# Performance work log

Measured on AMD Instinct MI355X. Metric: run time of the kernel, lower is better.

The kernel has to match this reference:

```python
import jax, jax.numpy as jnp
import numpy as np

B, S, E = 8, 2048, 512
VOCAB, FVOCAB = 32000, 128
SCALE = float(np.power(E, 0.5))  # emb_size ** (0.5 * temper), temper=1


def setup_inputs() -> dict:
    key = jax.random.key(0)
    ks = jax.random.split(key, 7)
    key_seq = jax.random.randint(ks[0], (B, S), 0, VOCAB, dtype=jnp.int32)
    value_seq = jax.random.randint(ks[1], (B, S), 0, FVOCAB, dtype=jnp.int32)
    hidden = jax.random.normal(ks[2], (B, S, E), dtype=jnp.float32)
    mask_matrix = jax.random.uniform(ks[3], (B, S, S), dtype=jnp.float32)
    nan_matrix = jnp.zeros((1,), dtype=jnp.int32)  # unused by forward
    # learned params; padding_idx=0 -> zero row in embeddings
    key_emb = jax.random.normal(ks[4], (VOCAB, E), dtype=jnp.float32).at[0].set(0.0)
    value_emb = jax.random.normal(ks[5], (FVOCAB, E), dtype=jnp.float32).at[0].set(0.0)
    weight = jax.random.normal(ks[6], (E, E), dtype=jnp.float32) / np.sqrt(E)
    return {
        "key_seq": key_seq, "value_seq": value_seq, "hidden": hidden,
        "mask_matrix": mask_matrix, "nan_matrix": nan_matrix,
        "key_emb": key_emb, "value_emb": value_emb, "weight": weight,
    }


def reference(key_seq, value_seq, hidden, mask_matrix, nan_matrix,
              key_emb, value_emb, weight):
    k = key_emb[key_seq]          # [B,S,E]
    v = value_emb[value_seq]      # [B,S,E]
    q = jnp.einsum('bsd,de->bse', hidden, weight)   # hidden @ weight
    u = jnp.einsum('bse,bte->bst', q, k) / SCALE    # QK^T, [B,S,S]
    mask = jnp.clip(mask_matrix.astype(u.dtype), 0.0, 1.0)
    exp_u = jnp.exp(u)
    delta = exp_u * mask
    p = delta / (jnp.sum(delta, axis=2, keepdims=True) + 1e-10)
    o = jnp.einsum('bst,bte->bse', p, v)            # PV, [B,S,E]
    return o
```

## Files before the change

kernel.cpp:

```cpp
#include <hip/hip_runtime.h>
#include <stdint.h>

#define BB 8
#define SS 2048
#define EE 512
#define INV_SCALE 0.04419417382415922f

typedef __attribute__((ext_vector_type(8))) short bf8_t;
typedef __attribute__((ext_vector_type(4))) float f4_t;

__device__ __forceinline__ unsigned short f2bf(float f) {
    union { float f; uint32_t u; } x; x.f = f;
    uint32_t r = x.u + 0x7fffu + ((x.u >> 16) & 1u);
    return (unsigned short)(r >> 16);
}


__global__ void __launch_bounds__(256) gather_k_kernel(const int* __restrict__ idx,
                                                       const float* __restrict__ emb,
                                                       unsigned short* __restrict__ out) {
    int id = blockIdx.x * 256 + threadIdx.x;
    int chunk = id & 63;
    int row = id >> 6;
    int e0 = chunk * 8;
    int k = idx[row];
    const float* src = emb + (size_t)k * EE + e0;
    float4 a = *(const float4*)(src);
    float4 c = *(const float4*)(src + 4);
    union { unsigned short s[8]; int4 v; } u;
    u.s[0] = f2bf(a.x); u.s[1] = f2bf(a.y); u.s[2] = f2bf(a.z); u.s[3] = f2bf(a.w);
    u.s[4] = f2bf(c.x); u.s[5] = f2bf(c.y); u.s[6] = f2bf(c.z); u.s[7] = f2bf(c.w);
    *(int4*)(out + (size_t)row * EE + e0) = u.v;
}

__global__ void __launch_bounds__(256) cast_h_kernel(const float* __restrict__ in,
                                                     unsigned short* __restrict__ out) {
    int id = blockIdx.x * 256 + threadIdx.x;
    const float* src = in + (size_t)id * 8;
    float4 a = *(const float4*)(src);
    float4 c = *(const float4*)(src + 4);
    union { unsigned short s[8]; int4 v; } u;
    u.s[0] = f2bf(a.x); u.s[1] = f2bf(a.y); u.s[2] = f2bf(a.z); u.s[3] = f2bf(a.w);
    u.s[4] = f2bf(c.x); u.s[5] = f2bf(c.y); u.s[6] = f2bf(c.z); u.s[7] = f2bf(c.w);
    *(int4*)(out + (size_t)id * 8) = u.v;
}

__global__ void __launch_bounds__(256) gather_vt_kernel(const int* __restrict__ idx,
                                                        const float* __restrict__ emb,
                                                        unsigned short* __restrict__ vt) {
    int id = blockIdx.x * 256 + threadIdx.x;
    int t = id & (SS - 1);
    int rest = id >> 11;
    int e = rest & (EE - 1);
    int b = rest >> 9;
    int k = idx[b * SS + t];
    vt[id] = f2bf(emb[(size_t)k * EE + e]);
}

__global__ void __launch_bounds__(256) transpose_w_kernel(const float* __restrict__ w,
                                                          unsigned short* __restrict__ wt) {
    int id = blockIdx.x * 256 + threadIdx.x;
    int e = id & (EE - 1);
    int f = id >> 9;
    wt[id] = f2bf(w[(size_t)e * EE + f] * INV_SCALE);
}


__device__ __forceinline__ void stage_tile(const unsigned short* gbase, int ld, int k0,
                                           unsigned short* lds, int wave, int lane) {
#pragma unroll
    for (int i = 0; i < 2; ++i) {
        int row = i * 64 + wave * 16 + (lane >> 2);
        int col = (lane & 3) * 8;
        const unsigned short* g = gbase + (size_t)row * ld + (k0 + col);
        unsigned short* l = lds + i * 2048 + wave * 512 + lane * 8;
        __builtin_amdgcn_global_load_lds((const __attribute__((address_space(1))) unsigned int*)g,
                                         (__attribute__((address_space(3))) unsigned int*)l,
                                         16, 0, 0);
    }
}

template <int KLEN>
__device__ __forceinline__ void mfma_loop(const unsigned short* Abase, int lda,
                                          const unsigned short* Bbase, int ldb,
                                          unsigned short* As, unsigned short* Bs,
                                          f4_t acc[4][4], int wave, int lane) {
    const int wm = wave >> 1, wn = wave & 1;
    const int quad = lane >> 4, l16 = lane & 15;
#pragma unroll 1
    for (int k0 = 0; k0 < KLEN; k0 += 32) {
        stage_tile(Abase, lda, k0, As, wave, lane);
        stage_tile(Bbase, ldb, k0, Bs, wave, lane);
        __syncthreads();
        bf8_t af[4], bfr[4];
#pragma unroll
        for (int mi = 0; mi < 4; ++mi)
            af[mi] = *(const bf8_t*)(As + (wm * 64 + mi * 16 + l16) * 32 + quad * 8);
#pragma unroll
        for (int ni = 0; ni < 4; ++ni)
            bfr[ni] = *(const bf8_t*)(Bs + (wn * 64 + ni * 16 + l16) * 32 + quad * 8);
#pragma unroll
        for (int mi = 0; mi < 4; ++mi)
#pragma unroll
            for (int ni = 0; ni < 4; ++ni)
                acc[mi][ni] = __builtin_amdgcn_mfma_f32_16x16x32_bf16(af[mi], bfr[ni],
                                                                      acc[mi][ni], 0, 0, 0);
        __syncthreads();
    }
}


__global__ void __launch_bounds__(256) qgen_kernel(const unsigned short* __restrict__ H,
                                                   const unsigned short* __restrict__ Wt,
                                                   unsigned short* __restrict__ Q) {
    __shared__ unsigned short As[128 * 32];
    __shared__ unsigned short Bs[128 * 32];
    const int tid = threadIdx.x, wave = tid >> 6, lane = tid & 63;
    const int rowT = blockIdx.y;
    const int colT = blockIdx.x;
    f4_t acc[4][4];
    const f4_t z = {0.f, 0.f, 0.f, 0.f};
    for (int i = 0; i < 4; ++i) for (int j = 0; j < 4; ++j) acc[i][j] = z;
    mfma_loop<EE>(H + (size_t)rowT * 128 * EE, EE,
                  Wt + (size_t)colT * 128 * EE, EE, As, Bs, acc, wave, lane);
    const int wm = wave >> 1, wn = wave & 1, quad = lane >> 4, l16 = lane & 15;
#pragma unroll
    for (int mi = 0; mi < 4; ++mi)
#pragma unroll
        for (int r = 0; r < 4; ++r) {
            int row = rowT * 128 + wm * 64 + mi * 16 + quad * 4 + r;
#pragma unroll
            for (int ni = 0; ni < 4; ++ni) {
                int col = colT * 128 + wn * 64 + ni * 16 + l16;
                Q[(size_t)row * EE + col] = f2bf(acc[mi][ni][r]);
            }
        }
}

__global__ void __launch_bounds__(256) qk_kernel(const unsigned short* __restrict__ Q,
                                                 const unsigned short* __restrict__ K,
                                                 const float* __restrict__ mask,
                                                 unsigned short* __restrict__ delta,
                                                 float* __restrict__ lsum) {
    __shared__ unsigned short As[128 * 32];
    __shared__ unsigned short Bs[128 * 32];
    const int tid = threadIdx.x, wave = tid >> 6, lane = tid & 63;
    const int b = blockIdx.z, qT = blockIdx.y, tT = blockIdx.x;
    f4_t acc[4][4];
    const f4_t z = {0.f, 0.f, 0.f, 0.f};
    for (int i = 0; i < 4; ++i) for (int j = 0; j < 4; ++j) acc[i][j] = z;
    mfma_loop<EE>(Q + ((size_t)b * SS + qT * 128) * EE, EE,
                  K + ((size_t)b * SS + tT * 128) * EE, EE, As, Bs, acc, wave, lane);
    const int wm = wave >> 1, wn = wave & 1, quad = lane >> 4, l16 = lane & 15;
#pragma unroll
    for (int mi = 0; mi < 4; ++mi)
#pragma unroll
        for (int r = 0; r < 4; ++r) {
            int row = qT * 128 + wm * 64 + mi * 16 + quad * 4 + r;
            const float* mrow = mask + ((size_t)b * SS + row) * SS;
            unsigned short* drow = delta + ((size_t)b * SS + row) * SS;
            float psum = 0.f;
#pragma unroll
            for (int ni = 0; ni < 4; ++ni) {
                int col = tT * 128 + wn * 64 + ni * 16 + l16;
                float m = mrow[col];
                m = fminf(fmaxf(m, 0.f), 1.f);
                float e = __expf(acc[mi][ni][r]) * m;
                drow[col] = f2bf(e);
                psum += e;
            }
#pragma unroll
            for (int off = 1; off < 16; off <<= 1)
                psum += __shfl_xor(psum, off, 16);
            if (l16 == 0) atomicAdd(&lsum[b * SS + row], psum);
        }
}

__global__ void __launch_bounds__(256) pv_kernel(const unsigned short* __restrict__ delta,
                                                 const unsigned short* __restrict__ Vt,
                                                 const float* __restrict__ lsum,
                                                 float* __restrict__ out) {
    __shared__ unsigned short As[128 * 32];
    __shared__ unsigned short Bs[128 * 32];
    const int tid = threadIdx.x, wave = tid >> 6, lane = tid & 63;
    const int b = blockIdx.z, qT = blockIdx.y, eT = blockIdx.x;
    f4_t acc[4][4];
    const f4_t z = {0.f, 0.f, 0.f, 0.f};
    for (int i = 0; i < 4; ++i) for (int j = 0; j < 4; ++j) acc[i][j] = z;
    mfma_loop<SS>(delta + ((size_t)b * SS + qT * 128) * SS, SS,
                  Vt + ((size_t)b * EE + eT * 128) * SS, SS, As, Bs, acc, wave, lane);
    const int wm = wave >> 1, wn = wave & 1, quad = lane >> 4, l16 = lane & 15;
#pragma unroll
    for (int mi = 0; mi < 4; ++mi)
#pragma unroll
        for (int r = 0; r < 4; ++r) {
            int row = qT * 128 + wm * 64 + mi * 16 + quad * 4 + r;
            float inv = 1.0f / (lsum[b * SS + row] + 1e-10f);
#pragma unroll
            for (int ni = 0; ni < 4; ++ni) {
                int col = eT * 128 + wn * 64 + ni * 16 + l16;
                out[((size_t)b * SS + row) * EE + col] = acc[mi][ni][r] * inv;
            }
        }
}


extern "C" void kernel_launch(void* const* d_in, const int* in_sizes, int n_in,
                              void* d_out, int out_size, void* d_ws, size_t ws_size,
                              hipStream_t stream) {
    const int*   key_seq = (const int*)d_in[0];
    const int*   val_seq = (const int*)d_in[1];
    const float* hidden  = (const float*)d_in[2];
    const float* mask    = (const float*)d_in[3];
    const float* key_emb = (const float*)d_in[5];
    const float* val_emb = (const float*)d_in[6];
    const float* weight  = (const float*)d_in[7];
    float* out = (float*)d_out;

    char* ws = (char*)d_ws;
    const size_t SZ_BSE = (size_t)BB * SS * EE * sizeof(unsigned short);
    unsigned short* Q    = (unsigned short*)(ws);
    unsigned short* K    = (unsigned short*)(ws + SZ_BSE);
    unsigned short* Vt   = (unsigned short*)(ws + 2 * SZ_BSE);
    unsigned short* H    = (unsigned short*)(ws + 3 * SZ_BSE);
    unsigned short* Wt   = (unsigned short*)(ws + 4 * SZ_BSE);
    float*          lsum = (float*)(ws + 4 * SZ_BSE + 524288);
    unsigned short* delta= (unsigned short*)(ws + 4 * SZ_BSE + 524288 + 65536);

    hipMemsetAsync(lsum, 0, (size_t)BB * SS * sizeof(float), stream);

    gather_k_kernel<<<4096, 256, 0, stream>>>(key_seq, key_emb, K);
    cast_h_kernel<<<4096, 256, 0, stream>>>(hidden, H);
    gather_vt_kernel<<<32768, 256, 0, stream>>>(val_seq, val_emb, Vt);
    transpose_w_kernel<<<1024, 256, 0, stream>>>(weight, Wt);

    qgen_kernel<<<dim3(4, 128), 256, 0, stream>>>(H, Wt, Q);
    qk_kernel<<<dim3(16, 16, 8), 256, 0, stream>>>(Q, K, mask, delta, lsum);
    pv_kernel<<<dim3(4, 16, 8), 256, 0, stream>>>(delta, Vt, lsum, out);
}
```

Before: 451.2 us.

## Double GEMM K-step, prefetch mask and lsum, vectorize V-transpose gather

Widens the shared-memory K tile from 32 to 64, halving the number of barrier pairs per GEMM at the cost of twice the LDS per block. The qk kernel now loads and clamps its mask values before the MFMA loop, packing them as bf16 in registers so those reads overlap the matmul, at the cost of extra register pressure and a bf16-rounded mask. The pv kernel loads its row sums and takes their reciprocals before its main loop. The V-transpose gather now has each thread produce 8 contiguous outputs with one 16-byte store, launching 8x fewer blocks.

Result: slower. 480.1 us (+6.4%).

```diff
diff --git a/kernel.cpp b/kernel.cpp
--- a/kernel.cpp
+++ b/kernel.cpp
@@ -13,6 +13,11 @@
     union { float f; uint32_t u; } x; x.f = f;
     uint32_t r = x.u + 0x7fffu + ((x.u >> 16) & 1u);
     return (unsigned short)(r >> 16);
+}
+
+__device__ __forceinline__ float bfbits2f(uint32_t hi_bits) {
+    union { uint32_t u; float f; } x; x.u = hi_bits;
+    return x.f;
 }
 
 
@@ -49,12 +54,24 @@
                                                         const float* __restrict__ emb,
                                                         unsigned short* __restrict__ vt) {
     int id = blockIdx.x * 256 + threadIdx.x;
-    int t = id & (SS - 1);
-    int rest = id >> 11;
+    int t8 = id & 255;
+    int rest = id >> 8;
     int e = rest & (EE - 1);
     int b = rest >> 9;
-    int k = idx[b * SS + t];
-    vt[id] = f2bf(emb[(size_t)k * EE + e]);
+    int t0 = t8 * 8;
+    const int* ip = idx + b * SS + t0;
+    int4 i0 = *(const int4*)(ip);
+    int4 i1 = *(const int4*)(ip + 4);
+    union { unsigned short s[8]; int4 v; } u;
+    u.s[0] = f2bf(emb[(size_t)i0.x * EE + e]);
+    u.s[1] = f2bf(emb[(size_t)i0.y * EE + e]);
+    u.s[2] = f2bf(emb[(size_t)i0.z * EE + e]);
+    u.s[3] = f2bf(emb[(size_t)i0.w * EE + e]);
+    u.s[4] = f2bf(emb[(size_t)i1.x * EE + e]);
+    u.s[5] = f2bf(emb[(size_t)i1.y * EE + e]);
+    u.s[6] = f2bf(emb[(size_t)i1.z * EE + e]);
+    u.s[7] = f2bf(emb[(size_t)i1.w * EE + e]);
+    *(int4*)(vt + ((size_t)b * EE + e) * SS + t0) = u.v;
 }
 
 __global__ void __launch_bounds__(256) transpose_w_kernel(const float* __restrict__ w,
@@ -66,12 +83,12 @@
 }
 
 
-__device__ __forceinline__ void stage_tile(const unsigned short* gbase, int ld, int k0,
-                                           unsigned short* lds, int wave, int lane) {
-#pragma unroll
-    for (int i = 0; i < 2; ++i) {
-        int row = i * 64 + wave * 16 + (lane >> 2);
-        int col = (lane & 3) * 8;
+__device__ __forceinline__ void stage_tile64(const unsigned short* gbase, int ld, int k0,
+                                             unsigned short* lds, int wave, int lane) {
+#pragma unroll
+    for (int i = 0; i < 4; ++i) {
+        int row = i * 32 + wave * 8 + (lane >> 3);
+        int col = (lane & 7) * 8;
         const unsigned short* g = gbase + (size_t)row * ld + (k0 + col);
         unsigned short* l = lds + i * 2048 + wave * 512 + lane * 8;
         __builtin_amdgcn_global_load_lds((const __attribute__((address_space(1))) unsigned int*)g,
@@ -88,23 +105,26 @@
     const int wm = wave >> 1, wn = wave & 1;
     const int quad = lane >> 4, l16 = lane & 15;
 #pragma unroll 1
-    for (int k0 = 0; k0 < KLEN; k0 += 32) {
-        stage_tile(Abase, lda, k0, As, wave, lane);
-        stage_tile(Bbase, ldb, k0, Bs, wave, lane);
+    for (int k0 = 0; k0 < KLEN; k0 += 64) {
+        stage_tile64(Abase, lda, k0, As, wave, lane);
+        stage_tile64(Bbase, ldb, k0, Bs, wave, lane);
         __syncthreads();
-        bf8_t af[4], bfr[4];
-#pragma unroll
-        for (int mi = 0; mi < 4; ++mi)
-            af[mi] = *(const bf8_t*)(As + (wm * 64 + mi * 16 + l16) * 32 + quad * 8);
-#pragma unroll
-        for (int ni = 0; ni < 4; ++ni)
-            bfr[ni] = *(const bf8_t*)(Bs + (wn * 64 + ni * 16 + l16) * 32 + quad * 8);
-#pragma unroll
-        for (int mi = 0; mi < 4; ++mi)
+#pragma unroll
+        for (int kk = 0; kk < 2; ++kk) {
+            bf8_t af[4], bfr[4];
+#pragma unroll
+            for (int mi = 0; mi < 4; ++mi)
+                af[mi] = *(const bf8_t*)(As + (wm * 64 + mi * 16 + l16) * 64 + kk * 32 + quad * 8);
 #pragma unroll
             for (int ni = 0; ni < 4; ++ni)
-                acc[mi][ni] = __builtin_amdgcn_mfma_f32_16x16x32_bf16(af[mi], bfr[ni],
-                                                                      acc[mi][ni], 0, 0, 0);
+                bfr[ni] = *(const bf8_t*)(Bs + (wn * 64 + ni * 16 + l16) * 64 + kk * 32 + quad * 8);
+#pragma unroll
+            for (int mi = 0; mi < 4; ++mi)
+#pragma unroll
+                for (int ni = 0; ni < 4; ++ni)
+                    acc[mi][ni] = __builtin_amdgcn_mfma_f32_16x16x32_bf16(af[mi], bfr[ni],
+                                                                          acc[mi][ni], 0, 0, 0);
+        }
         __syncthreads();
     }
 }
@@ -113,8 +133,8 @@
 __global__ void __launch_bounds__(256) qgen_kernel(const unsigned short* __restrict__ H,
                                                    const unsigned short* __restrict__ Wt,
                                                    unsigned short* __restrict__ Q) {
-    __shared__ unsigned short As[128 * 32];
-    __shared__ unsigned short Bs[128 * 32];
+    __shared__ unsigned short As[128 * 64];
+    __shared__ unsigned short Bs[128 * 64];
     const int tid = threadIdx.x, wave = tid >> 6, lane = tid & 63;
     const int rowT = blockIdx.y;
     const int colT = blockIdx.x;
@@ -142,32 +162,54 @@
                                                  const float* __restrict__ mask,
                                                  unsigned short* __restrict__ delta,
                                                  float* __restrict__ lsum) {
-    __shared__ unsigned short As[128 * 32];
-    __shared__ unsigned short Bs[128 * 32];
+    __shared__ unsigned short As[128 * 64];
+    __shared__ unsigned short Bs[128 * 64];
     const int tid = threadIdx.x, wave = tid >> 6, lane = tid & 63;
     const int b = blockIdx.z, qT = blockIdx.y, tT = blockIdx.x;
+    const int wm = wave >> 1, wn = wave & 1, quad = lane >> 4, l16 = lane & 15;
+
+    uint32_t mpk[4][4][2];
+#pragma unroll
+    for (int mi = 0; mi < 4; ++mi)
+#pragma unroll
+        for (int r = 0; r < 4; ++r) {
+            int row = qT * 128 + wm * 64 + mi * 16 + quad * 4 + r;
+            const float* mrow = mask + ((size_t)b * SS + row) * SS;
+#pragma unroll
+            for (int h = 0; h < 2; ++h) {
+                float m0 = mrow[tT * 128 + wn * 64 + (2 * h) * 16 + l16];
+                float m1 = mrow[tT * 128 + wn * 64 + (2 * h + 1) * 16 + l16];
+                m0 = fminf(fmaxf(m0, 0.f), 1.f);
+                m1 = fminf(fmaxf(m1, 0.f), 1.f);
+                mpk[mi][r][h] = (uint32_t)f2bf(m0) | ((uint32_t)f2bf(m1) << 16);
+            }
+        }
+
     f4_t acc[4][4];
     const f4_t z = {0.f, 0.f, 0.f, 0.f};
     for (int i = 0; i < 4; ++i) for (int j = 0; j < 4; ++j) acc[i][j] = z;
     mfma_loop<EE>(Q + ((size_t)b * SS + qT * 128) * EE, EE,
                   K + ((size_t)b * SS + tT * 128) * EE, EE, As, Bs, acc, wave, lane);
-    const int wm = wave >> 1, wn = wave & 1, quad = lane >> 4, l16 = lane & 15;
-#pragma unroll
-    for (int mi = 0; mi < 4; ++mi)
-#pragma unroll
-        for (int r = 0; r < 4; ++r) {
-            int row = qT * 128 + wm * 64 + mi * 16 + quad * 4 + r;
-            const float* mrow = mask + ((size_t)b * SS + row) * SS;
+
+#pragma unroll
+    for (int mi = 0; mi < 4; ++mi)
+#pragma unroll
+        for (int r = 0; r < 4; ++r) {
+            int row = qT * 128 + wm * 64 + mi * 16 + quad * 4 + r;
             unsigned short* drow = delta + ((size_t)b * SS + row) * SS;
             float psum = 0.f;
 #pragma unroll
-            for (int ni = 0; ni < 4; ++ni) {
-                int col = tT * 128 + wn * 64 + ni * 16 + l16;
-                float m = mrow[col];
-                m = fminf(fmaxf(m, 0.f), 1.f);
-                float e = __expf(acc[mi][ni][r]) * m;
-                drow[col] = f2bf(e);
-                psum += e;
+            for (int h = 0; h < 2; ++h) {
+                uint32_t pk = mpk[mi][r][h];
+                float mlo = bfbits2f(pk << 16);
+                float mhi = bfbits2f(pk & 0xffff0000u);
+                int col0 = tT * 128 + wn * 64 + (2 * h) * 16 + l16;
+                int col1 = col0 + 16;
+                float e0 = __expf(acc[mi][2 * h][r]) * mlo;
+                float e1 = __expf(acc[mi][2 * h + 1][r]) * mhi;
+                drow[col0] = f2bf(e0);
+                drow[col1] = f2bf(e1);
+                psum += e0 + e1;
             }
 #pragma unroll
             for (int off = 1; off < 16; off <<= 1)
@@ -180,26 +222,41 @@
                                                  const unsigned short* __restrict__ Vt,
                                                  const float* __restrict__ lsum,
                                                  float* __restrict__ out) {
-    __shared__ unsigned short As[128 * 32];
-    __shared__ unsigned short Bs[128 * 32];
+    __shared__ unsigned short As[128 * 64];
+    __shared__ unsigned short Bs[128 * 64];
     const int tid = threadIdx.x, wave = tid >> 6, lane = tid & 63;
     const int b = blockIdx.z, qT = blockIdx.y, eT = blockIdx.x;
+    const int wm = wave >> 1, wn = wave & 1, quad = lane >> 4, l16 = lane & 15;
+
+    float inv[4][4];
+#pragma unroll
+    for (int mi = 0; mi < 4; ++mi)
+#pragma unroll
+        for (int r = 0; r < 4; ++r) {
+            int row = qT * 128 + wm * 64 + mi * 16 + quad * 4 + r;
+            inv[mi][r] = lsum[b * SS + row];
+        }
+#pragma unroll
+    for (int mi = 0; mi < 4; ++mi)
+#pragma unroll
+        for (int r = 0; r < 4; ++r)
+            inv[mi][r] = 1.0f / (inv[mi][r] + 1e-10f);
+
     f4_t acc[4][4];
     const f4_t z = {0.f, 0.f, 0.f, 0.f};
     for (int i = 0; i < 4; ++i) for (int j = 0; j < 4; ++j) acc[i][j] = z;
     mfma_loop<SS>(delta + ((size_t)b * SS + qT * 128) * SS, SS,
                   Vt + ((size_t)b * EE + eT * 128) * SS, SS, As, Bs, acc, wave, lane);
-    const int wm = wave >> 1, wn = wave & 1, quad = lane >> 4, l16 = lane & 15;
-#pragma unroll
-    for (int mi = 0; mi < 4; ++mi)
-#pragma unroll
-        for (int r = 0; r < 4; ++r) {
-            int row = qT * 128 + wm * 64 + mi * 16 + quad * 4 + r;
-            float inv = 1.0f / (lsum[b * SS + row] + 1e-10f);
+
+#pragma unroll
+    for (int mi = 0; mi < 4; ++mi)
+#pragma unroll
+        for (int r = 0; r < 4; ++r) {
+            int row = qT * 128 + wm * 64 + mi * 16 + quad * 4 + r;
 #pragma unroll
             for (int ni = 0; ni < 4; ++ni) {
                 int col = eT * 128 + wn * 64 + ni * 16 + l16;
-                out[((size_t)b * SS + row) * EE + col] = acc[mi][ni][r] * inv;
+                out[((size_t)b * SS + row) * EE + col] = acc[mi][ni][r] * inv[mi][r];
             }
         }
 }
@@ -231,7 +288,7 @@
 
     gather_k_kernel<<<4096, 256, 0, stream>>>(key_seq, key_emb, K);
     cast_h_kernel<<<4096, 256, 0, stream>>>(hidden, H);
-    gather_vt_kernel<<<32768, 256, 0, stream>>>(val_seq, val_emb, Vt);
+    gather_vt_kernel<<<4096, 256, 0, stream>>>(val_seq, val_emb, Vt);
     transpose_w_kernel<<<1024, 256, 0, stream>>>(weight, Wt);
 
     qgen_kernel<<<dim3(4, 128), 256, 0, stream>>>(H, Wt, Q);
```

## Stream mask tile into LDS, restructure LDS staging layout, vectorize V gather

Applied to the files above, without the earlier changes.

The QK kernel now prefetches its 128x128 fp32 mask tile into shared memory with async global-to-LDS loads spread across the K loop. The scattered per-element mask reads in the epilogue become LDS reads. The GEMM staging layout changes so each wave loads a k-slice across 64 rows, and fragments are read from a quad-major LDS layout, aiming to cut bank conflicts. The transposed V gather writes 8 bf16 values per thread with vector index loads, and pv hoists the row-normalizer loads before the main loop. The added 64KB of shared memory in qk lowers occupancy.

Result: slower. 494.0 us (+9.5%).

```diff
diff --git a/kernel.cpp b/kernel.cpp
--- a/kernel.cpp
+++ b/kernel.cpp
@@ -49,12 +49,24 @@
                                                         const float* __restrict__ emb,
                                                         unsigned short* __restrict__ vt) {
     int id = blockIdx.x * 256 + threadIdx.x;
-    int t = id & (SS - 1);
-    int rest = id >> 11;
+    int t8 = id & 255;
+    int rest = id >> 8;
     int e = rest & (EE - 1);
     int b = rest >> 9;
-    int k = idx[b * SS + t];
-    vt[id] = f2bf(emb[(size_t)k * EE + e]);
+    int t0 = t8 * 8;
+    const int* ip = idx + b * SS + t0;
+    int4 i0 = *(const int4*)(ip);
+    int4 i1 = *(const int4*)(ip + 4);
+    union { unsigned short s[8]; int4 v; } u;
+    u.s[0] = f2bf(emb[(size_t)i0.x * EE + e]);
+    u.s[1] = f2bf(emb[(size_t)i0.y * EE + e]);
+    u.s[2] = f2bf(emb[(size_t)i0.z * EE + e]);
+    u.s[3] = f2bf(emb[(size_t)i0.w * EE + e]);
+    u.s[4] = f2bf(emb[(size_t)i1.x * EE + e]);
+    u.s[5] = f2bf(emb[(size_t)i1.y * EE + e]);
+    u.s[6] = f2bf(emb[(size_t)i1.z * EE + e]);
+    u.s[7] = f2bf(emb[(size_t)i1.w * EE + e]);
+    *(int4*)(vt + ((size_t)b * EE + e) * SS + t0) = u.v;
 }
 
 __global__ void __launch_bounds__(256) transpose_w_kernel(const float* __restrict__ w,
@@ -66,45 +78,49 @@
 }
 
 
-__device__ __forceinline__ void stage_tile(const unsigned short* gbase, int ld, int k0,
-                                           unsigned short* lds, int wave, int lane) {
-#pragma unroll
-    for (int i = 0; i < 2; ++i) {
-        int row = i * 64 + wave * 16 + (lane >> 2);
-        int col = (lane & 3) * 8;
-        const unsigned short* g = gbase + (size_t)row * ld + (k0 + col);
-        unsigned short* l = lds + i * 2048 + wave * 512 + lane * 8;
+__device__ __forceinline__ void stage128(const unsigned short* gbase, int ld,
+                                         unsigned short* lds, int wave, int lane) {
+#pragma unroll
+    for (int p = 0; p < 2; ++p) {
+        int row = p * 64 + lane;
+        const unsigned short* g = gbase + (size_t)row * ld + wave * 8;
+        unsigned short* l = lds + wave * 1024 + p * 512 + lane * 8;
         __builtin_amdgcn_global_load_lds((const __attribute__((address_space(1))) unsigned int*)g,
                                          (__attribute__((address_space(3))) unsigned int*)l,
                                          16, 0, 0);
     }
 }
 
+__device__ __forceinline__ void frag_mfma(const unsigned short* As, const unsigned short* Bs,
+                                          f4_t acc[4][4], int wm, int wn, int quad, int l16) {
+    bf8_t af[4], bfr[4];
+#pragma unroll
+    for (int mi = 0; mi < 4; ++mi)
+        af[mi] = *(const bf8_t*)(As + quad * 1024 + (wm * 64 + mi * 16 + l16) * 8);
+#pragma unroll
+    for (int ni = 0; ni < 4; ++ni)
+        bfr[ni] = *(const bf8_t*)(Bs + quad * 1024 + (wn * 64 + ni * 16 + l16) * 8);
+#pragma unroll
+    for (int mi = 0; mi < 4; ++mi)
+#pragma unroll
+        for (int ni = 0; ni < 4; ++ni)
+            acc[mi][ni] = __builtin_amdgcn_mfma_f32_16x16x32_bf16(af[mi], bfr[ni],
+                                                                  acc[mi][ni], 0, 0, 0);
+}
+
 template <int KLEN>
-__device__ __forceinline__ void mfma_loop(const unsigned short* Abase, int lda,
-                                          const unsigned short* Bbase, int ldb,
-                                          unsigned short* As, unsigned short* Bs,
-                                          f4_t acc[4][4], int wave, int lane) {
+__device__ __forceinline__ void mfma_loop_128(const unsigned short* Abase, int lda,
+                                              const unsigned short* Bbase, int ldb,
+                                              unsigned short* As, unsigned short* Bs,
+                                              f4_t acc[4][4], int wave, int lane) {
     const int wm = wave >> 1, wn = wave & 1;
     const int quad = lane >> 4, l16 = lane & 15;
 #pragma unroll 1
     for (int k0 = 0; k0 < KLEN; k0 += 32) {
-        stage_tile(Abase, lda, k0, As, wave, lane);
-        stage_tile(Bbase, ldb, k0, Bs, wave, lane);
-        __syncthreads();
-        bf8_t af[4], bfr[4];
-#pragma unroll
-        for (int mi = 0; mi < 4; ++mi)
-            af[mi] = *(const bf8_t*)(As + (wm * 64 + mi * 16 + l16) * 32 + quad * 8);
-#pragma unroll
-        for (int ni = 0; ni < 4; ++ni)
-            bfr[ni] = *(const bf8_t*)(Bs + (wn * 64 + ni * 16 + l16) * 32 + quad * 8);
-#pragma unroll
-        for (int mi = 0; mi < 4; ++mi)
-#pragma unroll
-            for (int ni = 0; ni < 4; ++ni)
-                acc[mi][ni] = __builtin_amdgcn_mfma_f32_16x16x32_bf16(af[mi], bfr[ni],
-                                                                      acc[mi][ni], 0, 0, 0);
+        stage128(Abase + k0, lda, As, wave, lane);
+        stage128(Bbase + k0, ldb, Bs, wave, lane);
+        __syncthreads();
+        frag_mfma(As, Bs, acc, wm, wn, quad, l16);
         __syncthreads();
     }
 }
@@ -121,8 +137,8 @@
     f4_t acc[4][4];
     const f4_t z = {0.f, 0.f, 0.f, 0.f};
     for (int i = 0; i < 4; ++i) for (int j = 0; j < 4; ++j) acc[i][j] = z;
-    mfma_loop<EE>(H + (size_t)rowT * 128 * EE, EE,
-                  Wt + (size_t)colT * 128 * EE, EE, As, Bs, acc, wave, lane);
+    mfma_loop_128<EE>(H + (size_t)rowT * 128 * EE, EE,
+                      Wt + (size_t)colT * 128 * EE, EE, As, Bs, acc, wave, lane);
     const int wm = wave >> 1, wn = wave & 1, quad = lane >> 4, l16 = lane & 15;
 #pragma unroll
     for (int mi = 0; mi < 4; ++mi)
@@ -144,29 +160,51 @@
                                                  float* __restrict__ lsum) {
     __shared__ unsigned short As[128 * 32];
     __shared__ unsigned short Bs[128 * 32];
+    __shared__ float Ms[128 * 128];
     const int tid = threadIdx.x, wave = tid >> 6, lane = tid & 63;
     const int b = blockIdx.z, qT = blockIdx.y, tT = blockIdx.x;
+    const int wm = wave >> 1, wn = wave & 1, quad = lane >> 4, l16 = lane & 15;
+
+    const unsigned short* Abase = Q + ((size_t)b * SS + qT * 128) * EE;
+    const unsigned short* Bbase = K + ((size_t)b * SS + tT * 128) * EE;
+    const float* mbase = mask + ((size_t)b * SS + qT * 128) * SS + tT * 128;
+
     f4_t acc[4][4];
     const f4_t z = {0.f, 0.f, 0.f, 0.f};
     for (int i = 0; i < 4; ++i) for (int j = 0; j < 4; ++j) acc[i][j] = z;
-    mfma_loop<EE>(Q + ((size_t)b * SS + qT * 128) * EE, EE,
-                  K + ((size_t)b * SS + tT * 128) * EE, EE, As, Bs, acc, wave, lane);
-    const int wm = wave >> 1, wn = wave & 1, quad = lane >> 4, l16 = lane & 15;
-#pragma unroll
-    for (int mi = 0; mi < 4; ++mi)
-#pragma unroll
-        for (int r = 0; r < 4; ++r) {
-            int row = qT * 128 + wm * 64 + mi * 16 + quad * 4 + r;
-            const float* mrow = mask + ((size_t)b * SS + row) * SS;
+
+#pragma unroll 1
+    for (int it = 0; it < 16; ++it) {
+        {
+            int g = it * 256 + tid;
+            const float* msrc = mbase + (size_t)(g >> 5) * SS + (g & 31) * 4;
+            float* mdst = Ms + (size_t)g * 4;
+            __builtin_amdgcn_global_load_lds((const __attribute__((address_space(1))) unsigned int*)msrc,
+                                             (__attribute__((address_space(3))) unsigned int*)mdst,
+                                             16, 0, 0);
+        }
+        stage128(Abase + it * 32, EE, As, wave, lane);
+        stage128(Bbase + it * 32, EE, Bs, wave, lane);
+        __syncthreads();
+        frag_mfma(As, Bs, acc, wm, wn, quad, l16);
+        __syncthreads();
+    }
+
+#pragma unroll
+    for (int mi = 0; mi < 4; ++mi)
+#pragma unroll
+        for (int r = 0; r < 4; ++r) {
+            int rloc = wm * 64 + mi * 16 + quad * 4 + r;
+            int row = qT * 128 + rloc;
             unsigned short* drow = delta + ((size_t)b * SS + row) * SS;
             float psum = 0.f;
 #pragma unroll
             for (int ni = 0; ni < 4; ++ni) {
-                int col = tT * 128 + wn * 64 + ni * 16 + l16;
-                float m = mrow[col];
+                int cloc = wn * 64 + ni * 16 + l16;
+                float m = Ms[rloc * 128 + cloc];
                 m = fminf(fmaxf(m, 0.f), 1.f);
                 float e = __expf(acc[mi][ni][r]) * m;
-                drow[col] = f2bf(e);
+                drow[tT * 128 + cloc] = f2bf(e);
                 psum += e;
             }
 #pragma unroll
@@ -184,22 +222,37 @@
     __shared__ unsigned short Bs[128 * 32];
     const int tid = threadIdx.x, wave = tid >> 6, lane = tid & 63;
     const int b = blockIdx.z, qT = blockIdx.y, eT = blockIdx.x;
+    const int wm = wave >> 1, wn = wave & 1, quad = lane >> 4, l16 = lane & 15;
+
+    float inv[4][4];
+#pragma unroll
+    for (int mi = 0; mi < 4; ++mi)
+#pragma unroll
+        for (int r = 0; r < 4; ++r) {
+            int row = qT * 128 + wm * 64 + mi * 16 + quad * 4 + r;
+            inv[mi][r] = lsum[b * SS + row];
+        }
+#pragma unroll
+    for (int mi = 0; mi < 4; ++mi)
+#pragma unroll
+        for (int r = 0; r < 4; ++r)
+            inv[mi][r] = 1.0f / (inv[mi][r] + 1e-10f);
+
     f4_t acc[4][4];
     const f4_t z = {0.f, 0.f, 0.f, 0.f};
     for (int i = 0; i < 4; ++i) for (int j = 0; j < 4; ++j) acc[i][j] = z;
-    mfma_loop<SS>(delta + ((size_t)b * SS + qT * 128) * SS, SS,
-                  Vt + ((size_t)b * EE + eT * 128) * SS, SS, As, Bs, acc, wave, lane);
-    const int wm = wave >> 1, wn = wave & 1, quad = lane >> 4, l16 = lane & 15;
+    mfma_loop_128<SS>(delta + ((size_t)b * SS + qT * 128) * SS, SS,
+                      Vt + ((size_t)b * EE + eT * 128) * SS, SS, As, Bs, acc, wave, lane);
+
 #pragma unroll
     for (int mi = 0; mi < 4; ++mi)
 #pragma unroll
         for (int r = 0; r < 4; ++r) {
             int row = qT * 128 + wm * 64 + mi * 16 + quad * 4 + r;
-            float inv = 1.0f / (lsum[b * SS + row] + 1e-10f);
 #pragma unroll
             for (int ni = 0; ni < 4; ++ni) {
                 int col = eT * 128 + wn * 64 + ni * 16 + l16;
-                out[((size_t)b * SS + row) * EE + col] = acc[mi][ni][r] * inv;
+                out[((size_t)b * SS + row) * EE + col] = acc[mi][ni][r] * inv[mi][r];
             }
         }
 }
@@ -231,7 +284,7 @@
 
     gather_k_kernel<<<4096, 256, 0, stream>>>(key_seq, key_emb, K);
     cast_h_kernel<<<4096, 256, 0, stream>>>(hidden, H);
-    gather_vt_kernel<<<32768, 256, 0, stream>>>(val_seq, val_emb, Vt);
+    gather_vt_kernel<<<4096, 256, 0, stream>>>(val_seq, val_emb, Vt);
     transpose_w_kernel<<<1024, 256, 0, stream>>>(weight, Wt);
 
     qgen_kernel<<<dim3(4, 128), 256, 0, stream>>>(H, Wt, Q);
```
